# Performance work log

Measured on AMD Instinct MI355X. Metric: run time of the kernel, lower is better.

## Reference

```python
import jax, jax.numpy as jnp
import numpy as np

B, S, E, H = 8, 1024, 768, 12
D = E // H  # per-head dim


def setup_inputs() -> dict:
    key = jax.random.key(0)
    ks = jax.random.split(key, 9)
    glorot = lambda k: jax.random.normal(k, (E, E), jnp.float32) * np.sqrt(2.0 / (E + E))
    return {
        "inputs": jax.random.normal(ks[0], (B, S, E), jnp.float32),
        "Wq": glorot(ks[1]), "bq": jnp.zeros((E,), jnp.float32),
        "Wk": glorot(ks[2]), "bk": jnp.zeros((E,), jnp.float32),
        "Wv": glorot(ks[3]), "bv": jnp.zeros((E,), jnp.float32),
        "Wo": glorot(ks[4]), "bo": jnp.zeros((E,), jnp.float32),
    }


def reference(inputs, Wq, bq, Wk, bk, Wv, bv, Wo, bo):
    b, s, e = inputs.shape
    # QKV projections then split heads: [B,S,E] -> [B,H,S,D]
    def heads(x):
        return x.reshape(b, s, H, D).transpose(0, 2, 1, 3)
    q = heads(inputs @ Wq + bq)
    k = heads(inputs @ Wk + bk)
    v = heads(inputs @ Wv + bv)
    scale = 1.0 / jnp.sqrt(jnp.asarray(D, inputs.dtype))
    scores = jnp.einsum("bhqd,bhkd->bhqk", q, k) * scale
    weights = jax.nn.softmax(scores, axis=-1)  # attn_drop rate 0 -> identity
    attn = jnp.einsum("bhqk,bhkd->bhqd", weights, v)
    concat = attn.transpose(0, 2, 1, 3).reshape(b, s, e)
    out = concat @ Wo + bo  # proj_drop rate 0 -> identity
    return out
```

## Files before the change

kernel.cpp:

```cpp
#include <hip/hip_runtime.h>
#include <math.h>

#define BB 8
#define SS 1024
#define EE 768
#define HH 12
#define DD 64
#define MM (BB*SS)

typedef __attribute__((ext_vector_type(8))) short short8;
typedef __attribute__((ext_vector_type(4))) short short4v;
typedef __attribute__((ext_vector_type(4))) float f32x4;

static __device__ __forceinline__ short f2bf(float x) {
    unsigned u = __float_as_uint(x);
    u += 0x7fffu + ((u >> 16) & 1u);
    return (short)(u >> 16);
}
static __device__ __forceinline__ short f2bf_fast(float x) {
    return (short)((__float_as_uint(x) + 0x8000u) >> 16);
}

static __device__ __forceinline__ void gload_lds16(const void* g, void* l) {
    __builtin_amdgcn_global_load_lds((__attribute__((address_space(1))) void*)g,
                                     (__attribute__((address_space(3))) void*)l,
                                     16, 0, 0);
}

__global__ __launch_bounds__(256)
void cast_x(const float* __restrict__ src, short* __restrict__ dst) {
    const long i = ((long)blockIdx.x * 256 + threadIdx.x) * 4;
    float4 v = *(const float4*)&src[i];
    short4v o;
    o.x = f2bf(v.x); o.y = f2bf(v.y); o.z = f2bf(v.z); o.w = f2bf(v.w);
    *(short4v*)&dst[i] = o;
}

__global__ __launch_bounds__(256)
void wcast_t(const float* __restrict__ W0, const float* __restrict__ W1,
             const float* __restrict__ W2, const float* __restrict__ W3,
             short* __restrict__ Wt) {
    __shared__ short T[64][72];
    const int z = blockIdx.z;
    const float* sp = (z == 0) ? W0 : (z == 1) ? W1 : (z == 2) ? W2 : W3;
    short* dp = Wt + (long)z * EE * EE;
    const int i0 = blockIdx.y * 64;
    const int j0 = blockIdx.x * 64;
    const int tid = threadIdx.x;
#pragma unroll
    for (int rep = 0; rep < 4; ++rep) {
        const int r = (tid >> 4) + rep * 16;
        const int c = (tid & 15) * 4;
        float4 v = *(const float4*)&sp[(long)(i0 + r) * EE + j0 + c];
        T[c + 0][r] = f2bf(v.x);
        T[c + 1][r] = f2bf(v.y);
        T[c + 2][r] = f2bf(v.z);
        T[c + 3][r] = f2bf(v.w);
    }
    __syncthreads();
#pragma unroll
    for (int rep = 0; rep < 4; ++rep) {
        const int rr = (tid >> 4) + rep * 16;
        const int cc = (tid & 15) * 4;
        short4v o;
        o.x = T[rr][cc + 0]; o.y = T[rr][cc + 1];
        o.z = T[rr][cc + 2]; o.w = T[rr][cc + 3];
        *(short4v*)&dp[(long)(j0 + rr) * EE + i0 + cc] = o;
    }
}

#define GEMM_CORE(Abase, Bbase, row0, col0)                                     \
    f32x4 acc[4][4];                                                            \
    _Pragma("unroll") for (int i = 0; i < 4; ++i)                               \
        _Pragma("unroll") for (int j = 0; j < 4; ++j)                           \
            acc[i][j] = (f32x4){0.f, 0.f, 0.f, 0.f};                            \
    const int rm = (w & 1) * 64, cn = (w >> 1) * 64;                            \
    for (int k0 = 0; k0 < EE; k0 += 64) {                                       \
        __syncthreads();                                                        \
        _Pragma("unroll") for (int i = 0; i < 4; ++i) {                         \
            const int chunk = w * 256 + i * 64 + lane;                          \
            const int r = chunk >> 3;                                           \
            const int cs = (((chunk & 7) ^ (r & 7)) << 3);                      \
            short* ldsA = Al + (w * 256 + i * 64) * 8;                          \
            short* ldsB = Bl + (w * 256 + i * 64) * 8;                          \
            gload_lds16(&Abase[(long)(row0 + r) * EE + k0 + cs], ldsA);         \
            gload_lds16(&Bbase[(long)(col0 + r) * EE + k0 + cs], ldsB);         \
        }                                                                       \
        __syncthreads();                                                        \
        _Pragma("unroll") for (int ks = 0; ks < 2; ++ks) {                      \
            short8 af[4], bf[4];                                                \
            _Pragma("unroll") for (int t = 0; t < 4; ++t)                       \
                af[t] = *(const short8*)&Al[(rm + t * 16 + m) * 64 +            \
                                            (((ks * 4 + quad) ^ (m & 7)) << 3)]; \
            _Pragma("unroll") for (int t = 0; t < 4; ++t)                       \
                bf[t] = *(const short8*)&Bl[(cn + t * 16 + m) * 64 +            \
                                            (((ks * 4 + quad) ^ (m & 7)) << 3)]; \
            _Pragma("unroll") for (int mt = 0; mt < 4; ++mt)                    \
                _Pragma("unroll") for (int nt = 0; nt < 4; ++nt)                \
                    acc[mt][nt] = __builtin_amdgcn_mfma_f32_16x16x32_bf16(      \
                        af[mt], bf[nt], acc[mt][nt], 0, 0, 0);                  \
        }                                                                       \
    }

#define TSTRIDE 134

#define QSCALE 0.1803368801111204f

__global__ __launch_bounds__(256)
void gemm_qkv(const short* __restrict__ Xb, const short* __restrict__ Wt,
              const float* __restrict__ bq, const float* __restrict__ bk,
              const float* __restrict__ bv,
              short* __restrict__ Qb, short* __restrict__ Kb,
              short* __restrict__ Vb) {
    __shared__ short SMEM[128 * TSTRIDE];
    short* const Al = SMEM;
    short* const Bl = SMEM + 128 * 64;
    const int tid = threadIdx.x, w = tid >> 6, lane = tid & 63;
    const int m = lane & 15, quad = lane >> 4;

    const int flat = blockIdx.x + 18 * blockIdx.y;
    const int id   = (flat & 7) * 144 + (flat >> 3);
    const int xcd  = id / 144;
    const int lcl  = id % 144;
    const int colw = lcl >> 3;
    const int wsel = colw / 6;
    const int colt = colw % 6;
    const int row0 = (xcd * 8 + (lcl & 7)) * 128;
    const int col0 = colt * 128;
    const short* Wsel = Wt + (long)wsel * EE * EE;
    const float* bias = (wsel == 0) ? bq : (wsel == 1) ? bk : bv;

    GEMM_CORE(Xb, Wsel, row0, col0)

    __syncthreads();
    const int b = row0 >> 10, s0 = row0 & 1023;

    if (wsel < 2) {
        const float scale = (wsel == 0) ? QSCALE : 1.0f;
        short* QK = (wsel == 0) ? Qb : Kb;
#pragma unroll
        for (int nt = 0; nt < 4; ++nt) {
            const float bvv = bias[col0 + cn + nt * 16 + m];
#pragma unroll
            for (int mt = 0; mt < 4; ++mt)
#pragma unroll
                for (int r = 0; r < 4; ++r)
                    SMEM[(rm + mt * 16 + quad * 4 + r) * TSTRIDE + cn + nt * 16 + m] =
                        f2bf((acc[mt][nt][r] + bvv) * scale);
        }
        __syncthreads();
#pragma unroll
        for (int rep = 0; rep < 8; ++rep) {
            const int chunk = tid + rep * 256;
            const int row = chunk >> 4;
            const int cc = (chunk & 15) * 8;
            const int colg = col0 + cc;
            const int h = colg >> 6, d = colg & 63;
            short8 v = *(const short8*)&SMEM[row * TSTRIDE + cc];
            *(short8*)&QK[((long)(b * HH + h) * SS + s0 + row) * DD + d] = v;
        }
    } else {
#pragma unroll
        for (int nt = 0; nt < 4; ++nt) {
            const float bvv = bias[col0 + cn + nt * 16 + m];
#pragma unroll
            for (int mt = 0; mt < 4; ++mt) {
                const int rowb = rm + mt * 16 + quad * 4;
                short4v o;
                o.x = f2bf(acc[mt][nt][0] + bvv);
                o.y = f2bf(acc[mt][nt][1] + bvv);
                o.z = f2bf(acc[mt][nt][2] + bvv);
                o.w = f2bf(acc[mt][nt][3] + bvv);
                *(short4v*)&SMEM[(cn + nt * 16 + m) * TSTRIDE + rowb] = o;
            }
        }
        __syncthreads();
#pragma unroll
        for (int rep = 0; rep < 8; ++rep) {
            const int chunk = tid + rep * 256;
            const int col = chunk >> 4;
            const int sc8 = (chunk & 15) * 8;
            const int colg = col0 + col;
            const int h = colg >> 6, d = colg & 63;
            short8 v = *(const short8*)&SMEM[col * TSTRIDE + sc8];
            *(short8*)&Vb[((long)(b * HH + h) * DD + d) * SS + s0 + sc8] = v;
        }
    }
}

__global__ __launch_bounds__(256)
void gemm_proj(const short* __restrict__ Cb, const short* __restrict__ WoT,
               const float* __restrict__ bo, float* __restrict__ out) {
    __shared__ short Al[128 * 64];
    __shared__ short Bl[128 * 64];
    const int tid = threadIdx.x, w = tid >> 6, lane = tid & 63;
    const int m = lane & 15, quad = lane >> 4;

    const int flat = blockIdx.x + 6 * blockIdx.y;
    const int id   = (flat & 7) * 48 + (flat >> 3);
    const int xcd  = id / 48;
    const int lcl  = id % 48;
    const int row0 = (xcd * 8 + (lcl & 7)) * 128;
    const int col0 = (lcl >> 3) * 128;

    GEMM_CORE(Cb, WoT, row0, col0)

#pragma unroll
    for (int nt = 0; nt < 4; ++nt) {
        const int colg = col0 + cn + nt * 16 + m;
        const float bvv = bo[colg];
#pragma unroll
        for (int mt = 0; mt < 4; ++mt)
#pragma unroll
            for (int r = 0; r < 4; ++r) {
                const int srow = row0 + rm + mt * 16 + quad * 4 + r;
                out[(long)srow * EE + colg] = acc[mt][nt][r] + bvv;
            }
    }
}


#define ATTN_STAGE(Kdst, Vdst, k0)                                            \
    do {                                                                      \
        _Pragma("unroll") for (int i = 0; i < 2; ++i) {                       \
            const int chunk = w * 128 + i * 64 + l;                           \
            const int r = chunk >> 3;                                         \
            const int cs = ((chunk & 7) ^ (r & 7)) << 3;                      \
            gload_lds16(&Kg[(long)((k0) + r) * DD + cs],                      \
                        (Kdst) + (w * 128 + i * 64) * 8);                     \
            gload_lds16(&Vg[(long)r * SS + (k0) + cs],                        \
                        (Vdst) + (w * 128 + i * 64) * 8);                     \
        }                                                                     \
    } while (0)

#define ATTN_COMPUTE(Kbuf, Vbuf)                                              \
    do {                                                                      \
        f32x4 sc[2][4];                                                       \
        __builtin_amdgcn_s_setprio(1);                                        \
        _Pragma("unroll") for (int nt = 0; nt < 4; ++nt) {                    \
            const short* kb = (Kbuf) + (nt * 16 + m) * 64;                    \
            short8 b0 = *(const short8*)&kb[(quad ^ (m & 7)) << 3];           \
            short8 b1 = *(const short8*)&kb[((4 + quad) ^ (m & 7)) << 3];     \
            _Pragma("unroll") for (int g = 0; g < 2; ++g) {                   \
                f32x4 a = (f32x4){0.f, 0.f, 0.f, 0.f};                        \
                a = __builtin_amdgcn_mfma_f32_16x16x32_bf16(aq[g][0], b0, a, 0, 0, 0); \
                a = __builtin_amdgcn_mfma_f32_16x16x32_bf16(aq[g][1], b1, a, 0, 0, 0); \
                sc[g][nt] = a;                                                \
            }                                                                 \
        }                                                                     \
        __builtin_amdgcn_s_setprio(0);                                        \
        _Pragma("unroll") for (int g = 0; g < 2; ++g)                         \
            _Pragma("unroll") for (int nt = 0; nt < 4; ++nt)                  \
                _Pragma("unroll") for (int r = 0; r < 4; ++r)                 \
                    sc[g][nt][r] = __builtin_amdgcn_exp2f(sc[g][nt][r]);      \
        short* Pw = Pl + w * 32 * 72;                                         \
        _Pragma("unroll") for (int g = 0; g < 2; ++g)                         \
            _Pragma("unroll") for (int nt = 0; nt < 4; ++nt)                  \
                _Pragma("unroll") for (int r = 0; r < 4; ++r)                 \
                    Pw[(g * 16 + quad * 4 + r) * 72 + nt * 16 + m] =          \
                        f2bf_fast(sc[g][nt][r]);                              \
        short8 ap[2][2];                                                      \
        _Pragma("unroll") for (int g = 0; g < 2; ++g) {                       \
            ap[g][0] = *(const short8*)(Pw + (g * 16 + m) * 72 + quad * 8);   \
            ap[g][1] = *(const short8*)(Pw + (g * 16 + m) * 72 + 32 + quad * 8); \
        }                                                                     \
        __builtin_amdgcn_s_setprio(1);                                        \
        _Pragma("unroll") for (int g = 0; g < 2; ++g) {                       \
            lacc[g] = __builtin_amdgcn_mfma_f32_16x16x32_bf16(ap[g][0], ones, lacc[g], 0, 0, 0); \
            lacc[g] = __builtin_amdgcn_mfma_f32_16x16x32_bf16(ap[g][1], ones, lacc[g], 0, 0, 0); \
        }                                                                     \
        _Pragma("unroll") for (int dt = 0; dt < 4; ++dt) {                    \
            const short* vb = (Vbuf) + (dt * 16 + m) * 64;                    \
            short8 b0 = *(const short8*)&vb[(quad ^ (m & 7)) << 3];           \
            short8 b1 = *(const short8*)&vb[((4 + quad) ^ (m & 7)) << 3];     \
            _Pragma("unroll") for (int g = 0; g < 2; ++g) {                   \
                O[g][dt] = __builtin_amdgcn_mfma_f32_16x16x32_bf16(ap[g][0], b0, O[g][dt], 0, 0, 0); \
                O[g][dt] = __builtin_amdgcn_mfma_f32_16x16x32_bf16(ap[g][1], b1, O[g][dt], 0, 0, 0); \
            }                                                                 \
        }                                                                     \
        __builtin_amdgcn_s_setprio(0);                                        \
    } while (0)

__global__ __launch_bounds__(256)
void attn_mfma(const short* __restrict__ Q,
               const short* __restrict__ K,
               const short* __restrict__ Vt,
               short* __restrict__ out) {
    __shared__ short K0l[64 * 64];
    __shared__ short K1l[64 * 64];
    __shared__ short V0l[64 * 64];
    __shared__ short V1l[64 * 64];
    __shared__ short Pl[4 * 32 * 72];

    const int tid  = threadIdx.x;
    const int w    = tid >> 6;
    const int l    = tid & 63;
    const int m    = l & 15;
    const int quad = l >> 4;

    const int flat = blockIdx.x + 8 * blockIdx.y + 96 * blockIdx.z;
    const int id   = (flat & 7) * 96 + (flat >> 3);
    const int qt   = id & 7;
    const int bh   = id >> 3;
    const int b    = bh / HH;
    const int h    = bh % HH;
    const int q0   = qt * 128;

    const short* Qg = Q  + (long)bh * SS * DD;
    const short* Kg = K  + (long)bh * SS * DD;
    const short* Vg = Vt + (long)bh * DD * SS;

    short8 aq[2][2];
#pragma unroll
    for (int g = 0; g < 2; ++g) {
        const int row = q0 + w * 32 + g * 16 + m;
        aq[g][0] = *(const short8*)(Qg + (long)row * DD + quad * 8);
        aq[g][1] = *(const short8*)(Qg + (long)row * DD + 32 + quad * 8);
    }

    short8 ones;
#pragma unroll
    for (int i = 0; i < 8; ++i) ones[i] = (short)0x3F80;

    f32x4 O[2][4], lacc[2];
#pragma unroll
    for (int g = 0; g < 2; ++g) {
        lacc[g] = (f32x4){0.f, 0.f, 0.f, 0.f};
#pragma unroll
        for (int dt = 0; dt < 4; ++dt) O[g][dt] = (f32x4){0.f, 0.f, 0.f, 0.f};
    }

    ATTN_STAGE(K0l, V0l, 0);
    __syncthreads();

#pragma unroll 1
    for (int kt2 = 0; kt2 < 8; ++kt2) {
        const int k0 = kt2 * 128;
        ATTN_STAGE(K1l, V1l, k0 + 64);
        ATTN_COMPUTE(K0l, V0l);
        __syncthreads();
        if (kt2 < 7) ATTN_STAGE(K0l, V0l, k0 + 128);
        ATTN_COMPUTE(K1l, V1l);
        __syncthreads();
    }

#pragma unroll
    for (int g = 0; g < 2; ++g)
#pragma unroll
        for (int r = 0; r < 4; ++r) {
            const float inv = 1.0f / lacc[g][r];
            const int qo = q0 + w * 32 + g * 16 + quad * 4 + r;
            short* orow = out + ((long)(b * SS + qo)) * EE + h * DD;
#pragma unroll
            for (int dt = 0; dt < 4; ++dt)
                orow[dt * 16 + m] = f2bf(O[g][dt][r] * inv);
        }
}

extern "C" void kernel_launch(void* const* d_in, const int* in_sizes, int n_in,
                              void* d_out, int out_size, void* d_ws, size_t ws_size,
                              hipStream_t stream) {
    const float* X  = (const float*)d_in[0];
    const float* Wq = (const float*)d_in[1];
    const float* bq = (const float*)d_in[2];
    const float* Wk = (const float*)d_in[3];
    const float* bk = (const float*)d_in[4];
    const float* Wv = (const float*)d_in[5];
    const float* bv = (const float*)d_in[6];
    const float* Wo = (const float*)d_in[7];
    const float* bo = (const float*)d_in[8];

    const long SEG = (long)BB * HH * SS * DD;
    const long WSEG = (long)EE * EE;
    short* Xb = (short*)d_ws;
    short* Wt = Xb + SEG;
    short* Qb = Wt + 4 * WSEG;
    short* Kb = Qb + SEG;
    short* Vb = Kb + SEG;
    short* Cb = Vb + SEG;

    cast_x<<<dim3(MM * EE / 4 / 256), 256, 0, stream>>>(X, Xb);
    wcast_t<<<dim3(12, 12, 4), 256, 0, stream>>>(Wq, Wk, Wv, Wo, Wt);

    gemm_qkv<<<dim3(18, 64), 256, 0, stream>>>(Xb, Wt, bq, bk, bv, Qb, Kb, Vb);

    attn_mfma<<<dim3(SS / 128, HH, BB), 256, 0, stream>>>(Qb, Kb, Vb, Cb);

    gemm_proj<<<dim3(6, 64), 256, 0, stream>>>(Cb, Wt + 3 * WSEG, bo,
                                               (float*)d_out);
}
```

Measured before the change: 206.7 us.

## Rewrite QKV GEMM as 256x256-tile, 8-wave kernel with double-buffered LDS pipeline

The QKV projection GEMM now uses 256x256 output tiles with 512 threads (8 waves in a 2x4 arrangement). LDS is double-buffered (even/odd stages) and global-to-LDS loads for the next K slices are interleaved with MFMA groups under explicit vmcnt waits and barriers, with raised wave priority around the MFMAs. This is meant to raise data reuse per tile and overlap memory latency with compute, where the old kernel synced around each single-buffered K step. The costs are 128KB of LDS, a large accumulator array that pressures registers, fewer blocks (288), and an epilogue split into two halves through shared memory.

New measurement: 209.8 us. No clear change (+1.5%).

```diff
diff --git a/kernel.cpp b/kernel.cpp
--- a/kernel.cpp
+++ b/kernel.cpp
@@ -26,6 +26,9 @@
                                      (__attribute__((address_space(3))) void*)l,
                                      16, 0, 0);
 }
+
+#define BAR __builtin_amdgcn_s_barrier()
+#define VMW(n) asm volatile("s_waitcnt vmcnt(" #n ")" ::: "memory")
 
 __global__ __launch_bounds__(256)
 void cast_x(const float* __restrict__ src, short* __restrict__ dst) {
@@ -79,7 +82,7 @@
         __syncthreads();                                                        \
         _Pragma("unroll") for (int i = 0; i < 4; ++i) {                         \
             const int chunk = w * 256 + i * 64 + lane;                          \
-            const int r = chunk >> 3;                                           \
+            const int r = chunk >> 3;                                          \
             const int cs = (((chunk & 7) ^ (r & 7)) << 3);                      \
             short* ldsA = Al + (w * 256 + i * 64) * 8;                          \
             short* ldsB = Bl + (w * 256 + i * 64) * 8;                          \
@@ -102,88 +105,200 @@
         }                                                                       \
     }
 
-#define TSTRIDE 134
-
 #define QSCALE 0.1803368801111204f
 
-__global__ __launch_bounds__(256)
+#define QKV_STG(Ld, Gbase, gr0, k0)                                           \
+    do {                                                                      \
+        _Pragma("unroll") for (int j = 0; j < 2; ++j) {                       \
+            const int chunk = j * 512 + tid;                                  \
+            const int r = chunk >> 3;                                         \
+            const int cs = ((chunk & 7) ^ (r & 7)) << 3;                      \
+            gload_lds16(&(Gbase)[(long)((gr0) + r) * EE + (k0) + cs],         \
+                        (Ld) + (j * 512 + w * 64) * 8);                       \
+        }                                                                     \
+    } while (0)
+
+#define QKV_RDA(Ld, mb)                                                       \
+    _Pragma("unroll") for (int t = 0; t < 4; ++t)                             \
+        _Pragma("unroll") for (int ks = 0; ks < 2; ++ks)                      \
+            af[t][ks] = *(const short8*)&(Ld)[(wr * 128 + ((mb) + t) * 16 + m) * 64 + \
+                                              (((ks * 4 + quad) ^ (m & 7)) << 3)];
+
+#define QKV_RDB(Ld, dst, nb)                                                  \
+    _Pragma("unroll") for (int t = 0; t < 2; ++t)                             \
+        _Pragma("unroll") for (int ks = 0; ks < 2; ++ks)                      \
+            dst[t][ks] = *(const short8*)&(Ld)[(wc * 64 + ((nb) + t) * 16 + m) * 64 + \
+                                               (((ks * 4 + quad) ^ (m & 7)) << 3)];
+
+#define QKV_MF(mb, bfx, nb)                                                   \
+    __builtin_amdgcn_s_setprio(1);                                            \
+    _Pragma("unroll") for (int mq = 0; mq < 4; ++mq)                          \
+        _Pragma("unroll") for (int nq = 0; nq < 2; ++nq)                      \
+            _Pragma("unroll") for (int ks = 0; ks < 2; ++ks)                  \
+                acc[(mb) + mq][(nb) + nq] = __builtin_amdgcn_mfma_f32_16x16x32_bf16( \
+                    af[mq][ks], bfx[nq][ks], acc[(mb) + mq][(nb) + nq], 0, 0, 0); \
+    __builtin_amdgcn_s_setprio(0);
+
+__global__ __launch_bounds__(512, 2)
 void gemm_qkv(const short* __restrict__ Xb, const short* __restrict__ Wt,
               const float* __restrict__ bq, const float* __restrict__ bk,
               const float* __restrict__ bv,
               short* __restrict__ Qb, short* __restrict__ Kb,
               short* __restrict__ Vb) {
-    __shared__ short SMEM[128 * TSTRIDE];
-    short* const Al = SMEM;
-    short* const Bl = SMEM + 128 * 64;
-    const int tid = threadIdx.x, w = tid >> 6, lane = tid & 63;
+    __shared__ short SMEM[65536];
+    short* const Ae = SMEM;
+    short* const Be = SMEM + 16384;
+    short* const Ao = SMEM + 32768;
+    short* const Bo = SMEM + 49152;
+
+    const int tid = threadIdx.x;
+    const int w = tid >> 6, lane = tid & 63;
     const int m = lane & 15, quad = lane >> 4;
-
-    const int flat = blockIdx.x + 18 * blockIdx.y;
-    const int id   = (flat & 7) * 144 + (flat >> 3);
-    const int xcd  = id / 144;
-    const int lcl  = id % 144;
-    const int colw = lcl >> 3;
-    const int wsel = colw / 6;
-    const int colt = colw % 6;
-    const int row0 = (xcd * 8 + (lcl & 7)) * 128;
-    const int col0 = colt * 128;
+    const int wr = w >> 2, wc = w & 3;
+
+    const int flat = blockIdx.x + 9 * blockIdx.y;
+    const int id   = (flat & 7) * 36 + (flat >> 3);
+    const int lcl  = id % 36;
+    const int rt   = (id / 36) * 4 + (lcl & 3);
+    const int ct   = lcl >> 2;
+    const int row0 = rt * 256;
+    const int col0 = ct * 256;
+    const int wsel = col0 / 768;
+    const int col0w = col0 % 768;
     const short* Wsel = Wt + (long)wsel * EE * EE;
     const float* bias = (wsel == 0) ? bq : (wsel == 1) ? bk : bv;
 
-    GEMM_CORE(Xb, Wsel, row0, col0)
-
+    f32x4 acc[8][4];
+#pragma unroll
+    for (int i = 0; i < 8; ++i)
+#pragma unroll
+        for (int j = 0; j < 4; ++j) acc[i][j] = (f32x4){0.f, 0.f, 0.f, 0.f};
+
+    QKV_STG(Ae + 0,    Xb,   row0 + 0,   0);
+    QKV_STG(Ae + 8192, Xb,   row0 + 128, 0);
+    QKV_STG(Be + 0,    Wsel, col0w + 0,   0);
+    QKV_STG(Be + 8192, Wsel, col0w + 128, 0);
+    QKV_STG(Bo + 0,    Wsel, col0w + 0,   64);
+    QKV_STG(Bo + 8192, Wsel, col0w + 128, 64);
+    VMW(4);
+    BAR;
+
+#pragma unroll 1
+    for (int it = 0; it < 6; ++it) {
+        const int kA = (2 * it + 1) * 64;
+        const int t2 = 2 * it + 2, t3 = 2 * it + 3;
+        const int k2 = (t2 < 12 ? t2 : 11) * 64;
+        const int k3 = (t3 < 12 ? t3 : 11) * 64;
+        short8 af[4][2], bf01[2][2], bf23[2][2];
+        QKV_RDA(Ae, 0);
+        QKV_RDB(Be, bf01, 0);
+        QKV_STG(Ao + 0, Xb, row0 + 0, kA);
+        BAR;
+        QKV_MF(0, bf01, 0);
+        BAR;
+        QKV_RDB(Be, bf23, 2);
+        QKV_STG(Ao + 8192, Xb, row0 + 128, kA);
+        BAR;
+        QKV_MF(0, bf23, 2);
+        BAR;
+        QKV_RDA(Ae, 4);
+        QKV_STG(Be + 0, Wsel, col0w + 0, k2);
+        BAR;
+        QKV_MF(4, bf01, 0);
+        BAR;
+        QKV_STG(Be + 8192, Wsel, col0w + 128, k2);
+        QKV_STG(Ae + 0,    Xb,   row0 + 0,   k2);
+        BAR;
+        QKV_MF(4, bf23, 2);
+        VMW(6);
+        BAR;
+        QKV_RDA(Ao, 0);
+        QKV_RDB(Bo, bf01, 0);
+        QKV_STG(Ae + 8192, Xb, row0 + 128, k2);
+        BAR;
+        QKV_MF(0, bf01, 0);
+        BAR;
+        QKV_RDB(Bo, bf23, 2);
+        BAR;
+        QKV_MF(0, bf23, 2);
+        BAR;
+        QKV_RDA(Ao, 4);
+        QKV_STG(Bo + 0, Wsel, col0w + 0, k3);
+        BAR;
+        QKV_MF(4, bf01, 0);
+        BAR;
+        QKV_STG(Bo + 8192, Wsel, col0w + 128, k3);
+        BAR;
+        QKV_MF(4, bf23, 2);
+        VMW(4);
+        BAR;
+    }
+
+    VMW(0);
     __syncthreads();
     const int b = row0 >> 10, s0 = row0 & 1023;
+    short* EP = SMEM;
 
     if (wsel < 2) {
         const float scale = (wsel == 0) ? QSCALE : 1.0f;
         short* QK = (wsel == 0) ? Qb : Kb;
-#pragma unroll
-        for (int nt = 0; nt < 4; ++nt) {
-            const float bvv = bias[col0 + cn + nt * 16 + m];
-#pragma unroll
-            for (int mt = 0; mt < 4; ++mt)
-#pragma unroll
-                for (int r = 0; r < 4; ++r)
-                    SMEM[(rm + mt * 16 + quad * 4 + r) * TSTRIDE + cn + nt * 16 + m] =
-                        f2bf((acc[mt][nt][r] + bvv) * scale);
-        }
-        __syncthreads();
-#pragma unroll
-        for (int rep = 0; rep < 8; ++rep) {
-            const int chunk = tid + rep * 256;
-            const int row = chunk >> 4;
-            const int cc = (chunk & 15) * 8;
-            const int colg = col0 + cc;
-            const int h = colg >> 6, d = colg & 63;
-            short8 v = *(const short8*)&SMEM[row * TSTRIDE + cc];
-            *(short8*)&QK[((long)(b * HH + h) * SS + s0 + row) * DD + d] = v;
+#pragma unroll 1
+        for (int hh = 0; hh < 2; ++hh) {
+            if (wr == hh) {
+#pragma unroll
+                for (int nt = 0; nt < 4; ++nt) {
+                    const float bvv = bias[col0w + wc * 64 + nt * 16 + m];
+#pragma unroll
+                    for (int mt = 0; mt < 8; ++mt)
+#pragma unroll
+                        for (int r = 0; r < 4; ++r)
+                            EP[(mt * 16 + quad * 4 + r) * 264 + wc * 64 + nt * 16 + m] =
+                                f2bf((acc[mt][nt][r] + bvv) * scale);
+                }
+            }
+            __syncthreads();
+#pragma unroll
+            for (int rep = 0; rep < 8; ++rep) {
+                const int chunk = tid + rep * 512;
+                const int row = chunk >> 5;
+                const int cc = (chunk & 31) * 8;
+                const int colg = col0w + cc;
+                const int h = colg >> 6, d = colg & 63;
+                short8 v = *(const short8*)&EP[row * 264 + cc];
+                *(short8*)&QK[((long)(b * HH + h) * SS + s0 + hh * 128 + row) * DD + d] = v;
+            }
+            __syncthreads();
         }
     } else {
-#pragma unroll
-        for (int nt = 0; nt < 4; ++nt) {
-            const float bvv = bias[col0 + cn + nt * 16 + m];
-#pragma unroll
-            for (int mt = 0; mt < 4; ++mt) {
-                const int rowb = rm + mt * 16 + quad * 4;
-                short4v o;
-                o.x = f2bf(acc[mt][nt][0] + bvv);
-                o.y = f2bf(acc[mt][nt][1] + bvv);
-                o.z = f2bf(acc[mt][nt][2] + bvv);
-                o.w = f2bf(acc[mt][nt][3] + bvv);
-                *(short4v*)&SMEM[(cn + nt * 16 + m) * TSTRIDE + rowb] = o;
+#pragma unroll 1
+        for (int hh = 0; hh < 2; ++hh) {
+            if (wr == hh) {
+#pragma unroll
+                for (int nt = 0; nt < 4; ++nt) {
+                    const float bvv = bias[col0w + wc * 64 + nt * 16 + m];
+#pragma unroll
+                    for (int mt = 0; mt < 8; ++mt) {
+                        short4v o;
+                        o.x = f2bf(acc[mt][nt][0] + bvv);
+                        o.y = f2bf(acc[mt][nt][1] + bvv);
+                        o.z = f2bf(acc[mt][nt][2] + bvv);
+                        o.w = f2bf(acc[mt][nt][3] + bvv);
+                        *(short4v*)&EP[(wc * 64 + nt * 16 + m) * 132 + mt * 16 + quad * 4] = o;
+                    }
+                }
             }
-        }
-        __syncthreads();
-#pragma unroll
-        for (int rep = 0; rep < 8; ++rep) {
-            const int chunk = tid + rep * 256;
-            const int col = chunk >> 4;
-            const int sc8 = (chunk & 15) * 8;
-            const int colg = col0 + col;
-            const int h = colg >> 6, d = colg & 63;
-            short8 v = *(const short8*)&SMEM[col * TSTRIDE + sc8];
-            *(short8*)&Vb[((long)(b * HH + h) * DD + d) * SS + s0 + sc8] = v;
+            __syncthreads();
+#pragma unroll
+            for (int rep = 0; rep < 8; ++rep) {
+                const int chunk = tid + rep * 512;
+                const int col = chunk >> 4;
+                const int sc8 = (chunk & 15) * 8;
+                const int colg = col0w + col;
+                const int h = colg >> 6, d = colg & 63;
+                short8 v = *(const short8*)&EP[col * 132 + sc8];
+                *(short8*)&Vb[((long)(b * HH + h) * DD + d) * SS + s0 + hh * 128 + sc8] = v;
+            }
+            __syncthreads();
         }
     }
 }
@@ -218,7 +333,6 @@
             }
     }
 }
-
 
 #define ATTN_STAGE(Kdst, Vdst, k0)                                            \
     do {                                                                      \
@@ -382,7 +496,7 @@
     cast_x<<<dim3(MM * EE / 4 / 256), 256, 0, stream>>>(X, Xb);
     wcast_t<<<dim3(12, 12, 4), 256, 0, stream>>>(Wq, Wk, Wv, Wo, Wt);
 
-    gemm_qkv<<<dim3(18, 64), 256, 0, stream>>>(Xb, Wt, bq, bk, bv, Qb, Kb, Vb);
+    gemm_qkv<<<dim3(9, 32), 512, 0, stream>>>(Xb, Wt, bq, bk, bv, Qb, Kb, Vb);
 
     attn_mfma<<<dim3(SS / 128, HH, BB), 256, 0, stream>>>(Qb, Kb, Vb, Cb);
 
```

## Rewrite QKV GEMM as 256x128-tile, 8-wave, double-buffered pipelined kernel

Applied to the files above, without the earlier changes.

Replaces the QKV projection GEMM's 128x128 tile with 256 threads by a 256x128 tile using 512 threads (8 waves, 2x4 layout). The main loop now double-buffers the A and B tiles in LDS (even/odd buffers) and interleaves global-to-LDS loads with MFMA work, using explicit vmcnt waits and raw barriers instead of full __syncthreads. The aim is to hide global load latency behind MFMA and to reuse each B tile over twice as many rows. The cost is 96KB of LDS, fragile hand-tuned wait counts, and a grid half the size of before.

After: 200.6 us. 1.03x faster.

```diff
diff --git a/kernel.cpp b/kernel.cpp
--- a/kernel.cpp
+++ b/kernel.cpp
@@ -26,6 +26,9 @@
                                      (__attribute__((address_space(3))) void*)l,
                                      16, 0, 0);
 }
+
+#define BAR __builtin_amdgcn_s_barrier()
+#define VMW(n) asm volatile("s_waitcnt vmcnt(" #n ")" ::: "memory")
 
 __global__ __launch_bounds__(256)
 void cast_x(const float* __restrict__ src, short* __restrict__ dst) {
@@ -79,7 +82,7 @@
         __syncthreads();                                                        \
         _Pragma("unroll") for (int i = 0; i < 4; ++i) {                         \
             const int chunk = w * 256 + i * 64 + lane;                          \
-            const int r = chunk >> 3;                                           \
+            const int r = chunk >> 3;                                          \
             const int cs = (((chunk & 7) ^ (r & 7)) << 3);                      \
             short* ldsA = Al + (w * 256 + i * 64) * 8;                          \
             short* ldsB = Bl + (w * 256 + i * 64) * 8;                          \
@@ -102,87 +105,179 @@
         }                                                                       \
     }
 
-#define TSTRIDE 134
-
 #define QSCALE 0.1803368801111204f
 
-__global__ __launch_bounds__(256)
+#define STG1(Ld, Gbase, gr0, k0)                                              \
+    do {                                                                      \
+        const int r_ = tid >> 3;                                              \
+        const int cs_ = ((tid & 7) ^ (r_ & 7)) << 3;                          \
+        gload_lds16(&(Gbase)[(long)((gr0) + r_) * EE + (k0) + cs_],           \
+                    (Ld) + w * 512);                                          \
+    } while (0)
+
+#define QKV_RDA(Ld, mb)                                                       \
+    _Pragma("unroll") for (int t = 0; t < 4; ++t)                             \
+        _Pragma("unroll") for (int ks = 0; ks < 2; ++ks)                      \
+            af[t][ks] = *(const short8*)&(Ld)[(wr * 128 + ((mb) + t) * 16 + m) * 64 + \
+                                              (((ks * 4 + quad) ^ (m & 7)) << 3)];
+
+#define QKV_RDB(Ld)                                                           \
+    _Pragma("unroll") for (int t = 0; t < 2; ++t)                             \
+        _Pragma("unroll") for (int ks = 0; ks < 2; ++ks)                      \
+            bf[t][ks] = *(const short8*)&(Ld)[(wc * 32 + t * 16 + m) * 64 +   \
+                                              (((ks * 4 + quad) ^ (m & 7)) << 3)];
+
+#define QKV_MF(mb)                                                            \
+    __builtin_amdgcn_s_setprio(1);                                            \
+    _Pragma("unroll") for (int mq = 0; mq < 4; ++mq)                          \
+        _Pragma("unroll") for (int nq = 0; nq < 2; ++nq)                      \
+            _Pragma("unroll") for (int ks = 0; ks < 2; ++ks)                  \
+                acc[(mb) + mq][nq] = __builtin_amdgcn_mfma_f32_16x16x32_bf16( \
+                    af[mq][ks], bf[nq][ks], acc[(mb) + mq][nq], 0, 0, 0);     \
+    __builtin_amdgcn_s_setprio(0);
+
+__global__ __launch_bounds__(512, 2)
 void gemm_qkv(const short* __restrict__ Xb, const short* __restrict__ Wt,
               const float* __restrict__ bq, const float* __restrict__ bk,
               const float* __restrict__ bv,
               short* __restrict__ Qb, short* __restrict__ Kb,
               short* __restrict__ Vb) {
-    __shared__ short SMEM[128 * TSTRIDE];
-    short* const Al = SMEM;
-    short* const Bl = SMEM + 128 * 64;
-    const int tid = threadIdx.x, w = tid >> 6, lane = tid & 63;
-    const int m = lane & 15, quad = lane >> 4;
+    __shared__ short SMEM[49152];
+    short* const Ae = SMEM;
+    short* const Ao = SMEM + 16384;
+    short* const Be = SMEM + 32768;
+    short* const Bo = SMEM + 40960;
+
+    const int tid = threadIdx.x;
+    const int w = tid >> 6;
+    const int m = tid & 15, quad = (tid & 63) >> 4;
+    const int wr = w >> 2, wc = w & 3;
 
     const int flat = blockIdx.x + 18 * blockIdx.y;
-    const int id   = (flat & 7) * 144 + (flat >> 3);
-    const int xcd  = id / 144;
-    const int lcl  = id % 144;
-    const int colw = lcl >> 3;
-    const int wsel = colw / 6;
-    const int colt = colw % 6;
-    const int row0 = (xcd * 8 + (lcl & 7)) * 128;
-    const int col0 = colt * 128;
+    const int id   = (flat & 7) * 72 + (flat >> 3);
+    const int lcl  = id % 72;
+    const int rt   = (id / 72) * 4 + (lcl & 3);
+    const int ct   = lcl >> 2;
+    const int row0 = rt * 256;
+    const int wsel = ct / 6;
+    const int col0w = (ct % 6) * 128;
     const short* Wsel = Wt + (long)wsel * EE * EE;
     const float* bias = (wsel == 0) ? bq : (wsel == 1) ? bk : bv;
 
-    GEMM_CORE(Xb, Wsel, row0, col0)
-
+    f32x4 acc[8][2];
+#pragma unroll
+    for (int i = 0; i < 8; ++i)
+#pragma unroll
+        for (int j = 0; j < 2; ++j) acc[i][j] = (f32x4){0.f, 0.f, 0.f, 0.f};
+
+    STG1(Ae + 0,     Xb,   row0 + 0,    0);
+    STG1(Ae + 8192,  Xb,   row0 + 128,  0);
+    STG1(Be + 0,     Wsel, col0w + 0,   0);
+    STG1(Be + 4096,  Wsel, col0w + 64,  0);
+    STG1(Ae + 4096,  Xb,   row0 + 64,   0);
+    STG1(Ae + 12288, Xb,   row0 + 192,  0);
+    STG1(Bo + 0,     Wsel, col0w + 0,   64);
+    STG1(Bo + 4096,  Wsel, col0w + 64,  64);
+    STG1(Ao + 0,     Xb,   row0 + 0,    64);
+    STG1(Ao + 8192,  Xb,   row0 + 128,  64);
+    VMW(6);
+    BAR;
+
+#pragma unroll 1
+    for (int it = 0; it < 6; ++it) {
+        const int kO1 = (2 * it + 1) * 64;
+        const int t2 = 2 * it + 2, t3 = 2 * it + 3;
+        const int kE2 = (t2 < 12 ? t2 : 11) * 64;
+        const int kO3 = (t3 < 12 ? t3 : 11) * 64;
+        short8 af[4][2], bf[2][2];
+        QKV_RDA(Ae, 0);
+        QKV_RDB(Be);
+        STG1(Ao + 4096,  Xb, row0 + 64,  kO1);
+        STG1(Ao + 12288, Xb, row0 + 192, kO1);
+        BAR;
+        QKV_MF(0);
+        VMW(6);
+        BAR;
+        QKV_RDA(Ae, 4);
+        STG1(Be + 0,     Wsel, col0w + 0,  kE2);
+        STG1(Be + 4096,  Wsel, col0w + 64, kE2);
+        STG1(Ae + 0,     Xb,   row0 + 0,   kE2);
+        STG1(Ae + 8192,  Xb,   row0 + 128, kE2);
+        BAR;
+        QKV_MF(4);
+        VMW(6);
+        BAR;
+        QKV_RDA(Ao, 0);
+        QKV_RDB(Bo);
+        STG1(Ae + 4096,  Xb, row0 + 64,  kE2);
+        STG1(Ae + 12288, Xb, row0 + 192, kE2);
+        BAR;
+        QKV_MF(0);
+        VMW(6);
+        BAR;
+        QKV_RDA(Ao, 4);
+        STG1(Bo + 0,     Wsel, col0w + 0,  kO3);
+        STG1(Bo + 4096,  Wsel, col0w + 64, kO3);
+        STG1(Ao + 0,     Xb,   row0 + 0,   kO3);
+        STG1(Ao + 8192,  Xb,   row0 + 128, kO3);
+        BAR;
+        QKV_MF(4);
+        VMW(6);
+        BAR;
+    }
+
+    VMW(0);
     __syncthreads();
     const int b = row0 >> 10, s0 = row0 & 1023;
+    short* EP = SMEM;
 
     if (wsel < 2) {
         const float scale = (wsel == 0) ? QSCALE : 1.0f;
         short* QK = (wsel == 0) ? Qb : Kb;
 #pragma unroll
-        for (int nt = 0; nt < 4; ++nt) {
-            const float bvv = bias[col0 + cn + nt * 16 + m];
-#pragma unroll
-            for (int mt = 0; mt < 4; ++mt)
+        for (int nt = 0; nt < 2; ++nt) {
+            const float bvv = bias[col0w + wc * 32 + nt * 16 + m];
+#pragma unroll
+            for (int mt = 0; mt < 8; ++mt)
 #pragma unroll
                 for (int r = 0; r < 4; ++r)
-                    SMEM[(rm + mt * 16 + quad * 4 + r) * TSTRIDE + cn + nt * 16 + m] =
+                    EP[(wr * 128 + mt * 16 + quad * 4 + r) * 136 + wc * 32 + nt * 16 + m] =
                         f2bf((acc[mt][nt][r] + bvv) * scale);
         }
         __syncthreads();
 #pragma unroll
         for (int rep = 0; rep < 8; ++rep) {
-            const int chunk = tid + rep * 256;
+            const int chunk = tid + rep * 512;
             const int row = chunk >> 4;
             const int cc = (chunk & 15) * 8;
-            const int colg = col0 + cc;
+            const int colg = col0w + cc;
             const int h = colg >> 6, d = colg & 63;
-            short8 v = *(const short8*)&SMEM[row * TSTRIDE + cc];
+            short8 v = *(const short8*)&EP[row * 136 + cc];
             *(short8*)&QK[((long)(b * HH + h) * SS + s0 + row) * DD + d] = v;
         }
     } else {
 #pragma unroll
-        for (int nt = 0; nt < 4; ++nt) {
-            const float bvv = bias[col0 + cn + nt * 16 + m];
-#pragma unroll
-            for (int mt = 0; mt < 4; ++mt) {
-                const int rowb = rm + mt * 16 + quad * 4;
+        for (int nt = 0; nt < 2; ++nt) {
+            const float bvv = bias[col0w + wc * 32 + nt * 16 + m];
+#pragma unroll
+            for (int mt = 0; mt < 8; ++mt) {
                 short4v o;
                 o.x = f2bf(acc[mt][nt][0] + bvv);
                 o.y = f2bf(acc[mt][nt][1] + bvv);
                 o.z = f2bf(acc[mt][nt][2] + bvv);
                 o.w = f2bf(acc[mt][nt][3] + bvv);
-                *(short4v*)&SMEM[(cn + nt * 16 + m) * TSTRIDE + rowb] = o;
+                *(short4v*)&EP[(wc * 32 + nt * 16 + m) * 264 + wr * 128 + mt * 16 + quad * 4] = o;
             }
         }
         __syncthreads();
 #pragma unroll
         for (int rep = 0; rep < 8; ++rep) {
-            const int chunk = tid + rep * 256;
-            const int col = chunk >> 4;
-            const int sc8 = (chunk & 15) * 8;
-            const int colg = col0 + col;
+            const int chunk = tid + rep * 512;
+            const int col = chunk >> 5;
+            const int sc8 = (chunk & 31) * 8;
+            const int colg = col0w + col;
             const int h = colg >> 6, d = colg & 63;
-            short8 v = *(const short8*)&SMEM[col * TSTRIDE + sc8];
+            short8 v = *(const short8*)&EP[col * 264 + sc8];
             *(short8*)&Vb[((long)(b * HH + h) * DD + d) * SS + s0 + sc8] = v;
         }
     }
@@ -218,7 +313,6 @@
             }
     }
 }
-
 
 #define ATTN_STAGE(Kdst, Vdst, k0)                                            \
     do {                                                                      \
@@ -382,7 +476,7 @@
     cast_x<<<dim3(MM * EE / 4 / 256), 256, 0, stream>>>(X, Xb);
     wcast_t<<<dim3(12, 12, 4), 256, 0, stream>>>(Wq, Wk, Wv, Wo, Wt);
 
-    gemm_qkv<<<dim3(18, 64), 256, 0, stream>>>(Xb, Wt, bq, bk, bv, Qb, Kb, Vb);
+    gemm_qkv<<<dim3(18, 32), 512, 0, stream>>>(Xb, Wt, bq, bk, bv, Qb, Kb, Vb);
 
     attn_mfma<<<dim3(SS / 128, HH, BB), 256, 0, stream>>>(Qb, Kb, Vb, Cb);
 
```
